# Kernel optimization log

Measured on AMD Instinct MI355X. Metric: run time of the kernel, lower is better.

## Reference

```python
import jax, jax.numpy as jnp
import numpy as np

N = 50000      # nodes
E = 800000     # edges
CIN = 128
CH = 128
COUT = 64
EPS = 1e-5     # BatchNorm eps


def setup_inputs() -> dict:
    key = jax.random.key(0)
    ks = jax.random.split(key, 16)
    s = 0.1  # weight scale for numerical stability
    return {
        "x": jax.random.normal(ks[0], (N, CIN), jnp.float32),
        "edge_index": jax.random.randint(ks[1], (2, E), 0, N, jnp.int32),
        "edge_weights": jax.random.uniform(ks[2], (E,), jnp.float32),
        "w1": jax.random.normal(ks[3], (CIN, CH), jnp.float32) * s,
        "b1": jnp.zeros((CH,), jnp.float32),
        "bn1_g": jnp.ones((CH,), jnp.float32),
        "bn1_b": jnp.zeros((CH,), jnp.float32),
        "bn1_m": jax.random.normal(ks[4], (CH,), jnp.float32) * 0.1,
        "bn1_v": jax.random.uniform(ks[5], (CH,), jnp.float32) + 0.5,
        "conv_ws": jax.random.normal(ks[6], (2, CH, CH), jnp.float32) * s,
        "conv_bs": jnp.zeros((2, CH), jnp.float32),
        "bns_g": jnp.ones((2, CH), jnp.float32),
        "bns_b": jnp.zeros((2, CH), jnp.float32),
        "bns_m": jax.random.normal(ks[7], (2, CH), jnp.float32) * 0.1,
        "bns_v": jax.random.uniform(ks[8], (2, CH), jnp.float32) + 0.5,
        "lin1_w": jax.random.normal(ks[9], (CH, CH), jnp.float32) * s,
        "lin1_b": jnp.zeros((CH,), jnp.float32),
        "lin2_w": jax.random.normal(ks[10], (CH, COUT), jnp.float32) * s,
        "lin2_b": jnp.zeros((COUT,), jnp.float32),
    }


def _bn(h, g, b, m, v):
    # BatchNorm1d in eval mode: running statistics
    return (h - m) * jax.lax.rsqrt(v + EPS) * g + b


def _gcn(h, w, b, src, dst, norm, n):
    # GCNConv: out[dst] += norm_e * (h @ W)[src]  (self loops already in src/dst)
    h = h @ w
    msg = h[src] * norm[:, None]                 # [E+N, CH]
    return jax.ops.segment_sum(msg, dst, num_segments=n) + b


def reference(x, edge_index, edge_weights, w1, b1, bn1_g, bn1_b, bn1_m, bn1_v,
              conv_ws, conv_bs, bns_g, bns_b, bns_m, bns_v,
              lin1_w, lin1_b, lin2_w, lin2_b):
    n = x.shape[0]
    loop = jnp.arange(n, dtype=edge_index.dtype)
    src = jnp.concatenate([edge_index[0], loop])
    dst = jnp.concatenate([edge_index[1], loop])
    ew = jnp.concatenate([edge_weights, jnp.ones((n,), edge_weights.dtype)])
    # symmetric degree normalization (PyG gcn_norm)
    deg = jax.ops.segment_sum(ew, dst, num_segments=n)
    dis = jnp.where(deg > 0, jax.lax.rsqrt(deg), 0.0)
    norm = dis[src] * ew * dis[dst]

    lrelu = jax.nn.leaky_relu  # slope 0.01, matches F.leaky_relu default
    h = lrelu(_bn(_gcn(x, w1, b1, src, dst, norm, n), bn1_g, bn1_b, bn1_m, bn1_v))
    for i in range(conv_ws.shape[0]):
        h = lrelu(_bn(_gcn(h, conv_ws[i], conv_bs[i], src, dst, norm, n),
                      bns_g[i], bns_b[i], bns_m[i], bns_v[i]) + h)
    h = lrelu(h @ lin1_w + lin1_b)
    # dropout is identity in eval mode
    return h @ lin2_w + lin2_b
```

## Files before the change

kernel.cpp:

```cpp
#include <hip/hip_runtime.h>
#include <hip/hip_bf16.h>


constexpr int   NN    = 50000;
constexpr int   EE    = 800000;
constexpr int   CH    = 128;
constexpr int   SLOTS = 64;
constexpr int   NBUK  = 782;
constexpr int   RCAP  = 2048;
constexpr int   EPB   = 4096;
constexpr float EPS   = 1e-5f;

typedef __attribute__((ext_vector_type(8))) short bf16x8;
typedef __attribute__((ext_vector_type(4))) float f32x4;
typedef unsigned long long u64;
typedef unsigned short u16;

__device__ inline u16 f2bf_rne(float f) {
  unsigned u = __float_as_uint(f);
  unsigned r = u + 0x7fffu + ((u >> 16) & 1u);
  return (u16)(r >> 16);
}
__device__ inline float bf2f(unsigned h16) {
  return __uint_as_float(h16 << 16);
}


__global__ __launch_bounds__(256) void bin_kernel(const int* __restrict__ ei,
                                                  const float* __restrict__ ew,
                                                  unsigned* __restrict__ gcur,
                                                  u64* __restrict__ bins) {
  __shared__ unsigned cnt[NBUK];
  __shared__ unsigned base[NBUK];
  const int tid = threadIdx.x;
  for (int b = tid; b < NBUK; b += 256) cnt[b] = 0;
  __syncthreads();
  const int e0 = blockIdx.x * EPB;
  unsigned pk[16]; u16 bkt[16]; u16 rnk[16]; unsigned char dl[16];
  #pragma unroll
  for (int i = 0; i < 16; i++) {
    int e = e0 + i * 256 + tid;
    if (e < EE) {
      int s = ei[e], d = ei[EE + e];
      float w = ew[e];
      bkt[i] = (u16)(d >> 6);
      dl[i]  = (unsigned char)(d & 63);
      pk[i]  = ((unsigned)f2bf_rne(w) << 16) | (unsigned)s;
      rnk[i] = (u16)atomicAdd(&cnt[bkt[i]], 1u);
    } else bkt[i] = 0xffffu;
  }
  __syncthreads();
  for (int b = tid; b < NBUK; b += 256) {
    unsigned c = cnt[b];
    base[b] = c ? atomicAdd(&gcur[b * 16], c) : 0u;
  }
  __syncthreads();
  #pragma unroll
  for (int i = 0; i < 16; i++) {
    if (bkt[i] == 0xffffu) continue;
    unsigned pos = base[bkt[i]] + rnk[i];
    if (pos < RCAP)
      bins[(size_t)bkt[i] * RCAP + pos] = ((u64)dl[i] << 32) | pk[i];
  }
}


__global__ __launch_bounds__(256) void scatter_kernel(const unsigned* __restrict__ gcur,
                                                      const u64* __restrict__ bins,
                                                      unsigned* __restrict__ ell,
                                                      float* __restrict__ dis) {
  __shared__ unsigned rank[64];
  __shared__ float    wsum[64];
  const int b   = blockIdx.x;
  const int tid = threadIdx.x;
  if (tid < 64) { rank[tid] = 1u; wsum[tid] = 0.f; }
  __syncthreads();
  unsigned cnt = gcur[b * 16];
  if (cnt > RCAP) cnt = RCAP;
  const u64* src = bins + (size_t)b * RCAP;
  for (unsigned i = tid; i < cnt; i += 256) {
    u64 v = src[i];
    unsigned pk = (unsigned)v;
    unsigned dl = (unsigned)(v >> 32);
    unsigned r = atomicAdd(&rank[dl], 1u);
    if (r < SLOTS)
      ell[((size_t)(b * 64 + dl)) * SLOTS + r] = pk;
    atomicAdd(&wsum[dl], bf2f(pk >> 16));
  }
  __syncthreads();
  if (tid < 64) {
    int node = b * 64 + tid;
    if (node < NN) {
      unsigned c = rank[tid];
      if (c > SLOTS) c = SLOTS;
      ell[(size_t)node * SLOTS] = c;
      dis[node] = rsqrtf(1.0f + wsum[tid]);
    }
  }
}

constexpr int NB_WZ = (73728 + 384 + 255) / 256;

__global__ void wswz_kernel(
    const float* __restrict__ w1, const float* __restrict__ bn1_g, const float* __restrict__ bn1_v,
    const float* __restrict__ conv_ws, const float* __restrict__ bns_g, const float* __restrict__ bns_v,
    const float* __restrict__ lin1_w, const float* __restrict__ lin2_w,
    const float* __restrict__ b1, const float* __restrict__ bn1_b, const float* __restrict__ bn1_m,
    const float* __restrict__ conv_bs, const float* __restrict__ bns_b, const float* __restrict__ bns_m,
    u16* __restrict__ w1h, u16* __restrict__ w1l,
    u16* __restrict__ c0h, u16* __restrict__ c0l,
    u16* __restrict__ c1h, u16* __restrict__ c1l,
    u16* __restrict__ l1h, u16* __restrict__ l1l,
    u16* __restrict__ l2h, u16* __restrict__ l2l,
    float* __restrict__ beff)
{
  int idx = blockIdx.x * 256 + threadIdx.x;
  if (idx >= 73728) {
    int r = idx - 73728;
    if (r >= 384) return;
    int l = r >> 7, c = r & 127;
    float bc, gg, bb, mm, vv;
    if (l == 0) { bc = b1[c]; gg = bn1_g[c]; bb = bn1_b[c]; mm = bn1_m[c]; vv = bn1_v[c]; }
    else {
      int o = (l - 1) * 128 + c;
      bc = conv_bs[o]; gg = bns_g[o]; bb = bns_b[o]; mm = bns_m[o]; vv = bns_v[o];
    }
    beff[r] = (bc - mm) * gg * rsqrtf(vv + EPS) + bb;
    return;
  }
  const float* W; const float* g = nullptr; const float* v = nullptr;
  u16 *hi, *lo; int CO = 128; int local;
  if      (idx < 16384) { W = w1;              g = bn1_g;     v = bn1_v;     hi = w1h; lo = w1l; local = idx; }
  else if (idx < 32768) { W = conv_ws;         g = bns_g;     v = bns_v;     hi = c0h; lo = c0l; local = idx - 16384; }
  else if (idx < 49152) { W = conv_ws + 16384; g = bns_g+128; v = bns_v+128; hi = c1h; lo = c1l; local = idx - 32768; }
  else if (idx < 65536) { W = lin1_w;                                        hi = l1h; lo = l1l; local = idx - 49152; }
  else                  { W = lin2_w;                                        hi = l2h; lo = l2l; local = idx - 65536; CO = 64; }
  int k = local / CO, n = local % CO;
  float w = W[local];
  if (g) w *= g[n] * rsqrtf(v[n] + EPS);
  int NCT = CO / 16;
  int kchunk = k >> 5, kin = k & 31, quad = kin >> 3, j = kin & 7;
  int ct = n >> 4, l = (quad << 4) | (n & 15);
  size_t pos = ((size_t)(kchunk * NCT + ct) * 64 + l) * 8 + j;
  u16 h = f2bf_rne(w);
  hi[pos] = h;
  lo[pos] = f2bf_rne(w - bf2f(h));
}

__global__ __launch_bounds__(256) void gemm1_kernel(
    const float* __restrict__ Ain,
    const u16* __restrict__ Whi, const u16* __restrict__ Wlo,
    const float* __restrict__ dis, u16* __restrict__ Cout)
{
  __shared__ float lds[64][CH + 4];
  const int tid  = threadIdx.x;
  const int wave = tid >> 6;
  const int lane = tid & 63;
  const int quad = lane >> 4;
  const int mrow = lane & 15;
  const int row0 = blockIdx.x * 64;

  int arow = row0 + wave * 16 + mrow;
  if (arow >= NN) arow = NN - 1;

  bf16x8 ahi[4], alo[4];
  const float* Ar = Ain + (size_t)arow * CH;
  #pragma unroll
  for (int c = 0; c < 4; c++) {
    int off = c * 32 + quad * 8;
    float4 f0 = *(const float4*)(Ar + off);
    float4 f1 = *(const float4*)(Ar + off + 4);
    float f[8] = {f0.x, f0.y, f0.z, f0.w, f1.x, f1.y, f1.z, f1.w};
    #pragma unroll
    for (int j = 0; j < 8; j++) {
      u16 h = f2bf_rne(f[j]);
      ahi[c][j] = (short)h;
      alo[c][j] = (short)f2bf_rne(f[j] - bf2f(h));
    }
  }

  f32x4 acc[8];
  #pragma unroll
  for (int t = 0; t < 8; t++) acc[t] = (f32x4){0.f, 0.f, 0.f, 0.f};
  #pragma unroll
  for (int c = 0; c < 4; c++) {
    #pragma unroll
    for (int t = 0; t < 8; t++) {
      size_t base = ((size_t)(c * 8 + t) * 64 + lane) * 8;
      bf16x8 bh = *(const bf16x8*)(Whi + base);
      bf16x8 bl = *(const bf16x8*)(Wlo + base);
      acc[t] = __builtin_amdgcn_mfma_f32_16x16x32_bf16(ahi[c], bh, acc[t], 0, 0, 0);
      acc[t] = __builtin_amdgcn_mfma_f32_16x16x32_bf16(alo[c], bh, acc[t], 0, 0, 0);
      acc[t] = __builtin_amdgcn_mfma_f32_16x16x32_bf16(ahi[c], bl, acc[t], 0, 0, 0);
    }
  }

  #pragma unroll
  for (int t = 0; t < 8; t++)
    #pragma unroll
    for (int r = 0; r < 4; r++)
      lds[wave * 16 + quad * 4 + r][t * 16 + mrow] = acc[t][r];
  __syncthreads();

  #pragma unroll
  for (int i = tid; i < 64 * CH / 4; i += 256) {
    int row = (i * 4) / CH;
    int col = (i * 4) % CH;
    int grow = row0 + row;
    if (grow >= NN) continue;
    float rs = dis[grow];
    const float* lp = &lds[row][col];
    u16* cp = (u16*)Cout + (size_t)grow * CH + col;
    unsigned p0 = ((unsigned)f2bf_rne(lp[1] * rs) << 16) | f2bf_rne(lp[0] * rs);
    unsigned p1 = ((unsigned)f2bf_rne(lp[3] * rs) << 16) | f2bf_rne(lp[2] * rs);
    *(uint2*)cp = make_uint2(p0, p1);
  }
}

template<bool RES>
__global__ __launch_bounds__(256, 5) void fuse_kernel(
    const u16* __restrict__ hwin,
    const unsigned* __restrict__ ell, const float* __restrict__ dis,
    const float* __restrict__ beff, const u16* __restrict__ res,
    const u16* __restrict__ Whi, const u16* __restrict__ Wlo,
    u16* __restrict__ hout, u16* __restrict__ hwout)
{
  __shared__ unsigned hs[64][68];
  const int tid  = threadIdx.x;
  const int wave = tid >> 6;
  const int lane = tid & 63;
  const int sub  = lane & 15;
  const int grp  = lane >> 4;
  const int row0 = blockIdx.x * 64;

  for (int r = 0; r < 16; r++) {
    int node = row0 + wave * 16 + r;
    int nd = node < NN ? node : NN - 1;
    unsigned myword = ell[(size_t)nd * SLOTS + lane];
    int cnt = __shfl((int)myword, 0);
    if (cnt > SLOTS) cnt = SLOTS;
    float a[8] = {0.f, 0.f, 0.f, 0.f, 0.f, 0.f, 0.f, 0.f};
    for (int j = 0; j < cnt; j += 16) {
      unsigned sidx[4]; float wv[4];
      #pragma unroll
      for (int q = 0; q < 4; q++) {
        int jj = j + q * 4 + grp;
        unsigned e = (unsigned)__shfl((int)myword, jj & 63);
        float    w = (jj == 0) ? 1.0f : bf2f(e >> 16);
        unsigned s = (jj == 0) ? (unsigned)nd : (e & 0xffffu);
        if (jj >= cnt) { w = 0.f; s = (unsigned)nd; }
        sidx[q] = s; wv[q] = w;
      }
      uint4 h[4];
      #pragma unroll
      for (int q = 0; q < 4; q++)
        h[q] = *(const uint4*)(hwin + (size_t)sidx[q] * CH + sub * 8);
      #pragma unroll
      for (int q = 0; q < 4; q++) {
        float w = wv[q];
        a[0] = fmaf(w, bf2f(h[q].x & 0xffffu), a[0]); a[1] = fmaf(w, bf2f(h[q].x >> 16), a[1]);
        a[2] = fmaf(w, bf2f(h[q].y & 0xffffu), a[2]); a[3] = fmaf(w, bf2f(h[q].y >> 16), a[3]);
        a[4] = fmaf(w, bf2f(h[q].z & 0xffffu), a[4]); a[5] = fmaf(w, bf2f(h[q].z >> 16), a[5]);
        a[6] = fmaf(w, bf2f(h[q].w & 0xffffu), a[6]); a[7] = fmaf(w, bf2f(h[q].w >> 16), a[7]);
      }
    }
    #pragma unroll
    for (int k = 0; k < 8; k++) {
      a[k] += __shfl_xor(a[k], 16);
      a[k] += __shfl_xor(a[k], 32);
    }
    if (grp == 0) {
      float disd = dis[nd];
      int c = sub * 8;
      float4 be0 = *(const float4*)(beff + c);
      float4 be1 = *(const float4*)(beff + c + 4);
      float y[8];
      y[0] = a[0] * disd + be0.x; y[1] = a[1] * disd + be0.y;
      y[2] = a[2] * disd + be0.z; y[3] = a[3] * disd + be0.w;
      y[4] = a[4] * disd + be1.x; y[5] = a[5] * disd + be1.y;
      y[6] = a[6] * disd + be1.z; y[7] = a[7] * disd + be1.w;
      if constexpr (RES) {
        uint4 rr = *(const uint4*)(res + (size_t)nd * CH + c);
        y[0] += bf2f(rr.x & 0xffffu); y[1] += bf2f(rr.x >> 16);
        y[2] += bf2f(rr.y & 0xffffu); y[3] += bf2f(rr.y >> 16);
        y[4] += bf2f(rr.z & 0xffffu); y[5] += bf2f(rr.z >> 16);
        y[6] += bf2f(rr.w & 0xffffu); y[7] += bf2f(rr.w >> 16);
      }
      #pragma unroll
      for (int k = 0; k < 8; k++) y[k] = y[k] > 0.f ? y[k] : 0.01f * y[k];
      uint4 o;
      o.x = ((unsigned)f2bf_rne(y[1]) << 16) | f2bf_rne(y[0]);
      o.y = ((unsigned)f2bf_rne(y[3]) << 16) | f2bf_rne(y[2]);
      o.z = ((unsigned)f2bf_rne(y[5]) << 16) | f2bf_rne(y[4]);
      o.w = ((unsigned)f2bf_rne(y[7]) << 16) | f2bf_rne(y[6]);
      if (node < NN) *(uint4*)(hout + (size_t)node * CH + c) = o;
      *(uint4*)&hs[wave * 16 + r][sub * 4] = o;
    }
  }

  bf16x8 af[4];
  #pragma unroll
  for (int c = 0; c < 4; c++)
    af[c] = *(const bf16x8*)&hs[wave * 16 + sub][c * 16 + grp * 4];

  f32x4 acc[8];
  #pragma unroll
  for (int t = 0; t < 8; t++) acc[t] = (f32x4){0.f, 0.f, 0.f, 0.f};
  #pragma unroll
  for (int c = 0; c < 4; c++) {
    #pragma unroll
    for (int t = 0; t < 8; t++) {
      size_t base = ((size_t)(c * 8 + t) * 64 + lane) * 8;
      bf16x8 bh = *(const bf16x8*)(Whi + base);
      bf16x8 bl = *(const bf16x8*)(Wlo + base);
      acc[t] = __builtin_amdgcn_mfma_f32_16x16x32_bf16(af[c], bh, acc[t], 0, 0, 0);
      acc[t] = __builtin_amdgcn_mfma_f32_16x16x32_bf16(af[c], bl, acc[t], 0, 0, 0);
    }
  }

  #pragma unroll
  for (int r = 0; r < 4; r++) {
    int grow = row0 + wave * 16 + grp * 4 + r;
    if (grow >= NN) continue;
    float rs = dis[grow];
    #pragma unroll
    for (int t = 0; t < 8; t++)
      hwout[(size_t)grow * CH + t * 16 + sub] = f2bf_rne(acc[t][r] * rs);
  }
}

__global__ __launch_bounds__(256, 4) void fuse_last_kernel(
    const u16* __restrict__ hwin,
    const unsigned* __restrict__ ell, const float* __restrict__ dis,
    const float* __restrict__ beff, const u16* __restrict__ res,
    const u16* __restrict__ l1h, const u16* __restrict__ l1l,
    const float* __restrict__ b1,
    const u16* __restrict__ l2h, const u16* __restrict__ l2l,
    const float* __restrict__ b2, float* __restrict__ out)
{
  __shared__ unsigned smem[64 * 132];
  float* fs = (float*)smem;
  const int tid  = threadIdx.x;
  const int wave = tid >> 6;
  const int lane = tid & 63;
  const int sub  = lane & 15;
  const int grp  = lane >> 4;
  const int row0 = blockIdx.x * 64;

  for (int r = 0; r < 16; r++) {
    int node = row0 + wave * 16 + r;
    int nd = node < NN ? node : NN - 1;
    unsigned myword = ell[(size_t)nd * SLOTS + lane];
    int cnt = __shfl((int)myword, 0);
    if (cnt > SLOTS) cnt = SLOTS;
    float a[8] = {0.f, 0.f, 0.f, 0.f, 0.f, 0.f, 0.f, 0.f};
    for (int j = 0; j < cnt; j += 16) {
      unsigned sidx[4]; float wv[4];
      #pragma unroll
      for (int q = 0; q < 4; q++) {
        int jj = j + q * 4 + grp;
        unsigned e = (unsigned)__shfl((int)myword, jj & 63);
        float    w = (jj == 0) ? 1.0f : bf2f(e >> 16);
        unsigned s = (jj == 0) ? (unsigned)nd : (e & 0xffffu);
        if (jj >= cnt) { w = 0.f; s = (unsigned)nd; }
        sidx[q] = s; wv[q] = w;
      }
      uint4 h[4];
      #pragma unroll
      for (int q = 0; q < 4; q++)
        h[q] = *(const uint4*)(hwin + (size_t)sidx[q] * CH + sub * 8);
      #pragma unroll
      for (int q = 0; q < 4; q++) {
        float w = wv[q];
        a[0] = fmaf(w, bf2f(h[q].x & 0xffffu), a[0]); a[1] = fmaf(w, bf2f(h[q].x >> 16), a[1]);
        a[2] = fmaf(w, bf2f(h[q].y & 0xffffu), a[2]); a[3] = fmaf(w, bf2f(h[q].y >> 16), a[3]);
        a[4] = fmaf(w, bf2f(h[q].z & 0xffffu), a[4]); a[5] = fmaf(w, bf2f(h[q].z >> 16), a[5]);
        a[6] = fmaf(w, bf2f(h[q].w & 0xffffu), a[6]); a[7] = fmaf(w, bf2f(h[q].w >> 16), a[7]);
      }
    }
    #pragma unroll
    for (int k = 0; k < 8; k++) {
      a[k] += __shfl_xor(a[k], 16);
      a[k] += __shfl_xor(a[k], 32);
    }
    if (grp == 0) {
      float disd = dis[nd];
      int c = sub * 8;
      float4 be0 = *(const float4*)(beff + c);
      float4 be1 = *(const float4*)(beff + c + 4);
      float y[8];
      y[0] = a[0] * disd + be0.x; y[1] = a[1] * disd + be0.y;
      y[2] = a[2] * disd + be0.z; y[3] = a[3] * disd + be0.w;
      y[4] = a[4] * disd + be1.x; y[5] = a[5] * disd + be1.y;
      y[6] = a[6] * disd + be1.z; y[7] = a[7] * disd + be1.w;
      uint4 rr = *(const uint4*)(res + (size_t)nd * CH + c);
      y[0] += bf2f(rr.x & 0xffffu); y[1] += bf2f(rr.x >> 16);
      y[2] += bf2f(rr.y & 0xffffu); y[3] += bf2f(rr.y >> 16);
      y[4] += bf2f(rr.z & 0xffffu); y[5] += bf2f(rr.z >> 16);
      y[6] += bf2f(rr.w & 0xffffu); y[7] += bf2f(rr.w >> 16);
      #pragma unroll
      for (int k = 0; k < 8; k++) y[k] = y[k] > 0.f ? y[k] : 0.01f * y[k];
      uint4 o;
      o.x = ((unsigned)f2bf_rne(y[1]) << 16) | f2bf_rne(y[0]);
      o.y = ((unsigned)f2bf_rne(y[3]) << 16) | f2bf_rne(y[2]);
      o.z = ((unsigned)f2bf_rne(y[5]) << 16) | f2bf_rne(y[4]);
      o.w = ((unsigned)f2bf_rne(y[7]) << 16) | f2bf_rne(y[6]);
      *(uint4*)&smem[(wave * 16 + r) * 68 + sub * 4] = o;
    }
  }

  bf16x8 af[4];
  #pragma unroll
  for (int c = 0; c < 4; c++)
    af[c] = *(const bf16x8*)&smem[(wave * 16 + sub) * 68 + c * 16 + grp * 4];
  __syncthreads();

  f32x4 acc[8];
  #pragma unroll
  for (int t = 0; t < 8; t++) acc[t] = (f32x4){0.f, 0.f, 0.f, 0.f};
  #pragma unroll
  for (int c = 0; c < 4; c++) {
    #pragma unroll
    for (int t = 0; t < 8; t++) {
      size_t base = ((size_t)(c * 8 + t) * 64 + lane) * 8;
      bf16x8 bh = *(const bf16x8*)(l1h + base);
      bf16x8 bl = *(const bf16x8*)(l1l + base);
      acc[t] = __builtin_amdgcn_mfma_f32_16x16x32_bf16(af[c], bh, acc[t], 0, 0, 0);
      acc[t] = __builtin_amdgcn_mfma_f32_16x16x32_bf16(af[c], bl, acc[t], 0, 0, 0);
    }
  }
  #pragma unroll
  for (int t = 0; t < 8; t++) {
    float bb = b1[t * 16 + sub];
    #pragma unroll
    for (int r = 0; r < 4; r++) {
      float x = acc[t][r] + bb;
      x = x > 0.f ? x : 0.01f * x;
      fs[(wave * 16 + grp * 4 + r) * 132 + t * 16 + sub] = x;
    }
  }

  f32x4 acc2[4];
  #pragma unroll
  for (int t = 0; t < 4; t++) acc2[t] = (f32x4){0.f, 0.f, 0.f, 0.f};
  #pragma unroll
  for (int c = 0; c < 4; c++) {
    bf16x8 ahi, alo;
    const float* lp = &fs[(wave * 16 + sub) * 132 + c * 32 + grp * 8];
    float4 f0 = *(const float4*)lp;
    float4 f1 = *(const float4*)(lp + 4);
    float f[8] = {f0.x, f0.y, f0.z, f0.w, f1.x, f1.y, f1.z, f1.w};
    #pragma unroll
    for (int j = 0; j < 8; j++) {
      u16 h = f2bf_rne(f[j]);
      ahi[j] = (short)h;
      alo[j] = (short)f2bf_rne(f[j] - bf2f(h));
    }
    #pragma unroll
    for (int t = 0; t < 4; t++) {
      size_t base = ((size_t)(c * 4 + t) * 64 + lane) * 8;
      bf16x8 bh = *(const bf16x8*)(l2h + base);
      bf16x8 bl = *(const bf16x8*)(l2l + base);
      acc2[t] = __builtin_amdgcn_mfma_f32_16x16x32_bf16(ahi, bh, acc2[t], 0, 0, 0);
      acc2[t] = __builtin_amdgcn_mfma_f32_16x16x32_bf16(alo, bh, acc2[t], 0, 0, 0);
      acc2[t] = __builtin_amdgcn_mfma_f32_16x16x32_bf16(ahi, bl, acc2[t], 0, 0, 0);
    }
  }
  #pragma unroll
  for (int t = 0; t < 4; t++) {
    float bb = b2[t * 16 + sub];
    #pragma unroll
    for (int r = 0; r < 4; r++) {
      int grow = row0 + wave * 16 + grp * 4 + r;
      if (grow < NN)
        out[(size_t)grow * 64 + t * 16 + sub] = acc2[t][r] + bb;
    }
  }
}


extern "C" void kernel_launch(void* const* d_in, const int* in_sizes, int n_in,
                              void* d_out, int out_size, void* d_ws, size_t ws_size,
                              hipStream_t stream) {
  const float* x       = (const float*)d_in[0];
  const int*   ei      = (const int*)  d_in[1];
  const float* ew      = (const float*)d_in[2];
  const float* w1      = (const float*)d_in[3];
  const float* b1      = (const float*)d_in[4];
  const float* bn1_g   = (const float*)d_in[5];
  const float* bn1_b   = (const float*)d_in[6];
  const float* bn1_m   = (const float*)d_in[7];
  const float* bn1_v   = (const float*)d_in[8];
  const float* conv_ws = (const float*)d_in[9];
  const float* conv_bs = (const float*)d_in[10];
  const float* bns_g   = (const float*)d_in[11];
  const float* bns_b   = (const float*)d_in[12];
  const float* bns_m   = (const float*)d_in[13];
  const float* bns_v   = (const float*)d_in[14];
  const float* lin1_w  = (const float*)d_in[15];
  const float* lin1_b  = (const float*)d_in[16];
  const float* lin2_w  = (const float*)d_in[17];
  const float* lin2_b  = (const float*)d_in[18];
  float* out = (float*)d_out;

  size_t off = 0;
  auto alloc = [&](size_t elems) -> void* {
    void* p = (char*)d_ws + off * 4;
    off += (elems + 3) & ~(size_t)3;
    return p;
  };
  unsigned* gcur = (unsigned*)alloc(NBUK * 16);
  u64*      bins = (u64*)     alloc((size_t)NBUK * RCAP * 2);
  unsigned* ell  = (unsigned*)alloc((size_t)NN * SLOTS);
  float*    dis  = (float*)   alloc(NN);
  float*    beff = (float*)   alloc(3 * CH);
  u16*      hwa  = (u16*)     alloc((size_t)NN * CH / 2);
  u16*      hwb  = (u16*)     alloc((size_t)NN * CH / 2);
  u16*      h1   = (u16*)     alloc((size_t)NN * CH / 2);
  u16*      h2   = (u16*)     alloc((size_t)NN * CH / 2);
  u16* w1h = (u16*)alloc(CH * CH / 2); u16* w1l = (u16*)alloc(CH * CH / 2);
  u16* c0h = (u16*)alloc(CH * CH / 2); u16* c0l = (u16*)alloc(CH * CH / 2);
  u16* c1h = (u16*)alloc(CH * CH / 2); u16* c1l = (u16*)alloc(CH * CH / 2);
  u16* l1h = (u16*)alloc(CH * CH / 2); u16* l1l = (u16*)alloc(CH * CH / 2);
  u16* l2h = (u16*)alloc(CH * 64 / 2); u16* l2l = (u16*)alloc(CH * 64 / 2);

  const int nb_bin  = (EE + EPB - 1) / EPB;
  const int nb_gemm = (NN + 63) / 64;
  dim3 B(256);

  hipMemsetAsync(gcur, 0, NBUK * 16 * sizeof(unsigned), stream);
  bin_kernel    <<<nb_bin, B, 0, stream>>>(ei, ew, gcur, bins);
  scatter_kernel<<<NBUK,   B, 0, stream>>>(gcur, bins, ell, dis);

  wswz_kernel<<<NB_WZ, B, 0, stream>>>(w1, bn1_g, bn1_v, conv_ws, bns_g, bns_v,
      lin1_w, lin2_w, b1, bn1_b, bn1_m, conv_bs, bns_b, bns_m,
      w1h, w1l, c0h, c0l, c1h, c1l, l1h, l1l, l2h, l2l, beff);

  gemm1_kernel<<<nb_gemm, B, 0, stream>>>(x, w1h, w1l, dis, hwa);

  fuse_kernel<false><<<nb_gemm, B, 0, stream>>>(hwa, ell, dis, beff, nullptr,
      c0h, c0l, h1, hwb);

  fuse_kernel<true><<<nb_gemm, B, 0, stream>>>(hwb, ell, dis, beff + CH, h1,
      c1h, c1l, h2, hwa);

  fuse_last_kernel<<<nb_gemm, B, 0, stream>>>(hwa, ell, dis, beff + 2 * CH, h2,
      l1h, l1l, lin1_b, l2h, l2l, lin2_b, out);
}
```

Before: 314.2 us.

## Switch to CSR adjacency and channel-sliced feature layout with split aggregate/GEMM kernels

Replaces the fixed 64-slot ELL adjacency with a compact CSR built through a new prefix-scan kernel. Features are stored in 8 channel slices of 16 bf16 each, so each aggregation block gathers a 32-byte slice per neighbour and the working set per slice is small enough to sit in cache. The fused aggregate+GEMM kernels are split into separate sagg, sgemm and linf kernels. This adds launches and extra global round trips for intermediates, in exchange for better gather locality and higher parallelism.

```diff
diff --git a/kernel.cpp b/kernel.cpp
--- a/kernel.cpp
+++ b/kernel.cpp
@@ -5,7 +5,6 @@
 constexpr int   NN    = 50000;
 constexpr int   EE    = 800000;
 constexpr int   CH    = 128;
-constexpr int   SLOTS = 64;
 constexpr int   NBUK  = 782;
 constexpr int   RCAP  = 2048;
 constexpr int   EPB   = 4096;
@@ -65,37 +64,80 @@
 }
 
 
+__global__ __launch_bounds__(256) void scan_kernel(const unsigned* __restrict__ gcur,
+                                                   unsigned* __restrict__ bbase) {
+  __shared__ unsigned lds[256];
+  __shared__ unsigned carry;
+  if (threadIdx.x == 0) carry = 0;
+  __syncthreads();
+  for (int base = 0; base < NBUK; base += 256) {
+    int i = base + threadIdx.x;
+    unsigned v = 0;
+    if (i < NBUK) { v = gcur[i * 16]; if (v > RCAP) v = RCAP; }
+    lds[threadIdx.x] = v;
+    __syncthreads();
+    for (int off = 1; off < 256; off <<= 1) {
+      unsigned t = (threadIdx.x >= off) ? lds[threadIdx.x - off] : 0u;
+      __syncthreads();
+      lds[threadIdx.x] += t;
+      __syncthreads();
+    }
+    if (i < NBUK) bbase[i] = carry + lds[threadIdx.x] - v;
+    __syncthreads();
+    if (threadIdx.x == 255) carry += lds[255];
+    __syncthreads();
+  }
+}
+
+
 __global__ __launch_bounds__(256) void scatter_kernel(const unsigned* __restrict__ gcur,
                                                       const u64* __restrict__ bins,
-                                                      unsigned* __restrict__ ell,
+                                                      const unsigned* __restrict__ bbase,
+                                                      unsigned* __restrict__ hdr,
+                                                      unsigned* __restrict__ edges,
                                                       float* __restrict__ dis) {
   __shared__ unsigned rank[64];
   __shared__ float    wsum[64];
+  __shared__ unsigned noff[64];
+  __shared__ unsigned rank2[64];
   const int b   = blockIdx.x;
   const int tid = threadIdx.x;
-  if (tid < 64) { rank[tid] = 1u; wsum[tid] = 0.f; }
+  if (tid < 64) { rank[tid] = 0u; wsum[tid] = 0.f; rank2[tid] = 0u; }
   __syncthreads();
   unsigned cnt = gcur[b * 16];
   if (cnt > RCAP) cnt = RCAP;
   const u64* src = bins + (size_t)b * RCAP;
   for (unsigned i = tid; i < cnt; i += 256) {
     u64 v = src[i];
-    unsigned pk = (unsigned)v;
     unsigned dl = (unsigned)(v >> 32);
-    unsigned r = atomicAdd(&rank[dl], 1u);
-    if (r < SLOTS)
-      ell[((size_t)(b * 64 + dl)) * SLOTS + r] = pk;
-    atomicAdd(&wsum[dl], bf2f(pk >> 16));
+    atomicAdd(&rank[dl], 1u);
+    atomicAdd(&wsum[dl], bf2f(((unsigned)v) >> 16));
+  }
+  __syncthreads();
+  if (tid == 0) {
+    unsigned acc = bbase[b];
+    #pragma unroll 1
+    for (int k = 0; k < 64; k++) {
+      noff[k] = acc;
+      unsigned c = rank[k]; if (c > 63u) c = 63u;
+      acc += c;
+    }
   }
   __syncthreads();
   if (tid < 64) {
     int node = b * 64 + tid;
     if (node < NN) {
-      unsigned c = rank[tid];
-      if (c > SLOTS) c = SLOTS;
-      ell[(size_t)node * SLOTS] = c;
+      unsigned c = rank[tid]; if (c > 63u) c = 63u;
+      hdr[node] = (noff[tid] << 6) | c;
       dis[node] = rsqrtf(1.0f + wsum[tid]);
     }
+  }
+  __syncthreads();
+  for (unsigned i = tid; i < cnt; i += 256) {
+    u64 v = src[i];
+    unsigned dl = (unsigned)(v >> 32);
+    unsigned r = atomicAdd(&rank2[dl], 1u);
+    if (r < 63u) edges[noff[dl] + r] = (unsigned)v;
   }
 }
 
@@ -202,76 +244,81 @@
       lds[wave * 16 + quad * 4 + r][t * 16 + mrow] = acc[t][r];
   __syncthreads();
 
-  #pragma unroll
-  for (int i = tid; i < 64 * CH / 4; i += 256) {
-    int row = (i * 4) / CH;
-    int col = (i * 4) % CH;
+  for (int i = tid; i < 64 * 8; i += 256) {
+    int row = i >> 3, slice = i & 7;
     int grow = row0 + row;
     if (grow >= NN) continue;
     float rs = dis[grow];
-    const float* lp = &lds[row][col];
-    u16* cp = (u16*)Cout + (size_t)grow * CH + col;
-    unsigned p0 = ((unsigned)f2bf_rne(lp[1] * rs) << 16) | f2bf_rne(lp[0] * rs);
-    unsigned p1 = ((unsigned)f2bf_rne(lp[3] * rs) << 16) | f2bf_rne(lp[2] * rs);
-    *(uint2*)cp = make_uint2(p0, p1);
+    const float* lp = &lds[row][slice * 16];
+    u16* cp = Cout + ((size_t)slice * NN + grow) * 16;
+    uint4 o0, o1;
+    o0.x = ((unsigned)f2bf_rne(lp[1] * rs) << 16) | f2bf_rne(lp[0] * rs);
+    o0.y = ((unsigned)f2bf_rne(lp[3] * rs) << 16) | f2bf_rne(lp[2] * rs);
+    o0.z = ((unsigned)f2bf_rne(lp[5] * rs) << 16) | f2bf_rne(lp[4] * rs);
+    o0.w = ((unsigned)f2bf_rne(lp[7] * rs) << 16) | f2bf_rne(lp[6] * rs);
+    o1.x = ((unsigned)f2bf_rne(lp[9] * rs) << 16) | f2bf_rne(lp[8] * rs);
+    o1.y = ((unsigned)f2bf_rne(lp[11] * rs) << 16) | f2bf_rne(lp[10] * rs);
+    o1.z = ((unsigned)f2bf_rne(lp[13] * rs) << 16) | f2bf_rne(lp[12] * rs);
+    o1.w = ((unsigned)f2bf_rne(lp[15] * rs) << 16) | f2bf_rne(lp[14] * rs);
+    *(uint4*)cp = o0;
+    *(uint4*)(cp + 8) = o1;
   }
 }
 
 template<bool RES>
-__global__ __launch_bounds__(256, 5) void fuse_kernel(
-    const u16* __restrict__ hwin,
-    const unsigned* __restrict__ ell, const float* __restrict__ dis,
+__global__ __launch_bounds__(256) void sagg_kernel(
+    const u16* __restrict__ hw, const unsigned* __restrict__ hdr,
+    const unsigned* __restrict__ edges, const float* __restrict__ dis,
     const float* __restrict__ beff, const u16* __restrict__ res,
-    const u16* __restrict__ Whi, const u16* __restrict__ Wlo,
-    u16* __restrict__ hout, u16* __restrict__ hwout)
+    u16* __restrict__ hout)
 {
-  __shared__ unsigned hs[64][68];
-  const int tid  = threadIdx.x;
-  const int wave = tid >> 6;
-  const int lane = tid & 63;
-  const int sub  = lane & 15;
-  const int grp  = lane >> 4;
-  const int row0 = blockIdx.x * 64;
+  const int blk   = blockIdx.x;
+  const int slice = blk & 7;
+  const int tile  = blk >> 3;
+  const int wave  = threadIdx.x >> 6;
+  const int lane  = threadIdx.x & 63;
+  const int half  = lane & 1;
+  const int eid   = lane >> 1;
+  const u16* hws  = hw + (size_t)slice * NN * 16;
 
   for (int r = 0; r < 16; r++) {
-    int node = row0 + wave * 16 + r;
+    int node = tile * 64 + wave * 16 + r;
     int nd = node < NN ? node : NN - 1;
-    unsigned myword = ell[(size_t)nd * SLOTS + lane];
-    int cnt = __shfl((int)myword, 0);
-    if (cnt > SLOTS) cnt = SLOTS;
+    unsigned h = hdr[nd];
+    unsigned off = h >> 6;
+    int cnt = (int)(h & 63u);
+
     float a[8] = {0.f, 0.f, 0.f, 0.f, 0.f, 0.f, 0.f, 0.f};
-    for (int j = 0; j < cnt; j += 16) {
-      unsigned sidx[4]; float wv[4];
-      #pragma unroll
-      for (int q = 0; q < 4; q++) {
-        int jj = j + q * 4 + grp;
-        unsigned e = (unsigned)__shfl((int)myword, jj & 63);
-        float    w = (jj == 0) ? 1.0f : bf2f(e >> 16);
-        unsigned s = (jj == 0) ? (unsigned)nd : (e & 0xffffu);
-        if (jj >= cnt) { w = 0.f; s = (unsigned)nd; }
-        sidx[q] = s; wv[q] = w;
+    for (int jb = 0; jb < cnt; jb += 32) {
+      int jj = jb + eid;
+      if (jj < cnt) {
+        unsigned e = edges[off + jj];
+        float w = bf2f(e >> 16);
+        unsigned s = e & 0xffffu;
+        uint4 hv = *(const uint4*)(hws + (size_t)s * 16 + half * 8);
+        a[0] = fmaf(w, bf2f(hv.x & 0xffffu), a[0]); a[1] = fmaf(w, bf2f(hv.x >> 16), a[1]);
+        a[2] = fmaf(w, bf2f(hv.y & 0xffffu), a[2]); a[3] = fmaf(w, bf2f(hv.y >> 16), a[3]);
+        a[4] = fmaf(w, bf2f(hv.z & 0xffffu), a[4]); a[5] = fmaf(w, bf2f(hv.z >> 16), a[5]);
+        a[6] = fmaf(w, bf2f(hv.w & 0xffffu), a[6]); a[7] = fmaf(w, bf2f(hv.w >> 16), a[7]);
       }
-      uint4 h[4];
-      #pragma unroll
-      for (int q = 0; q < 4; q++)
-        h[q] = *(const uint4*)(hwin + (size_t)sidx[q] * CH + sub * 8);
-      #pragma unroll
-      for (int q = 0; q < 4; q++) {
-        float w = wv[q];
-        a[0] = fmaf(w, bf2f(h[q].x & 0xffffu), a[0]); a[1] = fmaf(w, bf2f(h[q].x >> 16), a[1]);
-        a[2] = fmaf(w, bf2f(h[q].y & 0xffffu), a[2]); a[3] = fmaf(w, bf2f(h[q].y >> 16), a[3]);
-        a[4] = fmaf(w, bf2f(h[q].z & 0xffffu), a[4]); a[5] = fmaf(w, bf2f(h[q].z >> 16), a[5]);
-        a[6] = fmaf(w, bf2f(h[q].w & 0xffffu), a[6]); a[7] = fmaf(w, bf2f(h[q].w >> 16), a[7]);
-      }
     }
     #pragma unroll
     for (int k = 0; k < 8; k++) {
+      a[k] += __shfl_xor(a[k], 2);
+      a[k] += __shfl_xor(a[k], 4);
+      a[k] += __shfl_xor(a[k], 8);
       a[k] += __shfl_xor(a[k], 16);
       a[k] += __shfl_xor(a[k], 32);
     }
-    if (grp == 0) {
+
+    if (lane < 2 && node < NN) {
+      uint4 sv = *(const uint4*)(hws + (size_t)nd * 16 + half * 8);
+      a[0] += bf2f(sv.x & 0xffffu); a[1] += bf2f(sv.x >> 16);
+      a[2] += bf2f(sv.y & 0xffffu); a[3] += bf2f(sv.y >> 16);
+      a[4] += bf2f(sv.z & 0xffffu); a[5] += bf2f(sv.z >> 16);
+      a[6] += bf2f(sv.w & 0xffffu); a[7] += bf2f(sv.w >> 16);
       float disd = dis[nd];
-      int c = sub * 8;
+      int c = slice * 16 + half * 8;
       float4 be0 = *(const float4*)(beff + c);
       float4 be1 = *(const float4*)(beff + c + 4);
       float y[8];
@@ -280,7 +327,7 @@
       y[4] = a[4] * disd + be1.x; y[5] = a[5] * disd + be1.y;
       y[6] = a[6] * disd + be1.z; y[7] = a[7] * disd + be1.w;
       if constexpr (RES) {
-        uint4 rr = *(const uint4*)(res + (size_t)nd * CH + c);
+        uint4 rr = *(const uint4*)(res + ((size_t)slice * NN + nd) * 16 + half * 8);
         y[0] += bf2f(rr.x & 0xffffu); y[1] += bf2f(rr.x >> 16);
         y[2] += bf2f(rr.y & 0xffffu); y[3] += bf2f(rr.y >> 16);
         y[4] += bf2f(rr.z & 0xffffu); y[5] += bf2f(rr.z >> 16);
@@ -293,15 +340,33 @@
       o.y = ((unsigned)f2bf_rne(y[3]) << 16) | f2bf_rne(y[2]);
       o.z = ((unsigned)f2bf_rne(y[5]) << 16) | f2bf_rne(y[4]);
       o.w = ((unsigned)f2bf_rne(y[7]) << 16) | f2bf_rne(y[6]);
-      if (node < NN) *(uint4*)(hout + (size_t)node * CH + c) = o;
-      *(uint4*)&hs[wave * 16 + r][sub * 4] = o;
-    }
-  }
+      *(uint4*)(hout + ((size_t)slice * NN + node) * 16 + half * 8) = o;
+    }
+  }
+}
+
+__global__ __launch_bounds__(256) void sgemm_kernel(
+    const u16* __restrict__ Ain,
+    const u16* __restrict__ Whi, const u16* __restrict__ Wlo,
+    const float* __restrict__ dis, u16* __restrict__ Cout)
+{
+  const int tid  = threadIdx.x;
+  const int wave = tid >> 6;
+  const int lane = tid & 63;
+  const int quad = lane >> 4;
+  const int mrow = lane & 15;
+  const int row0 = blockIdx.x * 64;
+
+  int arow = row0 + wave * 16 + mrow;
+  if (arow >= NN) arow = NN - 1;
 
   bf16x8 af[4];
   #pragma unroll
-  for (int c = 0; c < 4; c++)
-    af[c] = *(const bf16x8*)&hs[wave * 16 + sub][c * 16 + grp * 4];
+  for (int c = 0; c < 4; c++) {
+    int slice = 2 * c + (quad >> 1);
+    int off = (quad & 1) * 8;
+    af[c] = *(const bf16x8*)(Ain + ((size_t)slice * NN + arow) * 16 + off);
+  }
 
   f32x4 acc[8];
   #pragma unroll
@@ -320,100 +385,40 @@
 
   #pragma unroll
   for (int r = 0; r < 4; r++) {
-    int grow = row0 + wave * 16 + grp * 4 + r;
+    int grow = row0 + wave * 16 + quad * 4 + r;
     if (grow >= NN) continue;
     float rs = dis[grow];
     #pragma unroll
     for (int t = 0; t < 8; t++)
-      hwout[(size_t)grow * CH + t * 16 + sub] = f2bf_rne(acc[t][r] * rs);
-  }
-}
-
-__global__ __launch_bounds__(256, 4) void fuse_last_kernel(
-    const u16* __restrict__ hwin,
-    const unsigned* __restrict__ ell, const float* __restrict__ dis,
-    const float* __restrict__ beff, const u16* __restrict__ res,
+      Cout[((size_t)t * NN + grow) * 16 + mrow] = f2bf_rne(acc[t][r] * rs);
+  }
+}
+
+__global__ __launch_bounds__(256) void linf_kernel(
+    const u16* __restrict__ Ain,
     const u16* __restrict__ l1h, const u16* __restrict__ l1l,
     const float* __restrict__ b1,
     const u16* __restrict__ l2h, const u16* __restrict__ l2l,
     const float* __restrict__ b2, float* __restrict__ out)
 {
-  __shared__ unsigned smem[64 * 132];
-  float* fs = (float*)smem;
+  __shared__ float fs[64 * 132];
   const int tid  = threadIdx.x;
   const int wave = tid >> 6;
   const int lane = tid & 63;
-  const int sub  = lane & 15;
-  const int grp  = lane >> 4;
+  const int quad = lane >> 4;
+  const int mrow = lane & 15;
   const int row0 = blockIdx.x * 64;
 
-  for (int r = 0; r < 16; r++) {
-    int node = row0 + wave * 16 + r;
-    int nd = node < NN ? node : NN - 1;
-    unsigned myword = ell[(size_t)nd * SLOTS + lane];
-    int cnt = __shfl((int)myword, 0);
-    if (cnt > SLOTS) cnt = SLOTS;
-    float a[8] = {0.f, 0.f, 0.f, 0.f, 0.f, 0.f, 0.f, 0.f};
-    for (int j = 0; j < cnt; j += 16) {
-      unsigned sidx[4]; float wv[4];
-      #pragma unroll
-      for (int q = 0; q < 4; q++) {
-        int jj = j + q * 4 + grp;
-        unsigned e = (unsigned)__shfl((int)myword, jj & 63);
-        float    w = (jj == 0) ? 1.0f : bf2f(e >> 16);
-        unsigned s = (jj == 0) ? (unsigned)nd : (e & 0xffffu);
-        if (jj >= cnt) { w = 0.f; s = (unsigned)nd; }
-        sidx[q] = s; wv[q] = w;
-      }
-      uint4 h[4];
-      #pragma unroll
-      for (int q = 0; q < 4; q++)
-        h[q] = *(const uint4*)(hwin + (size_t)sidx[q] * CH + sub * 8);
-      #pragma unroll
-      for (int q = 0; q < 4; q++) {
-        float w = wv[q];
-        a[0] = fmaf(w, bf2f(h[q].x & 0xffffu), a[0]); a[1] = fmaf(w, bf2f(h[q].x >> 16), a[1]);
-        a[2] = fmaf(w, bf2f(h[q].y & 0xffffu), a[2]); a[3] = fmaf(w, bf2f(h[q].y >> 16), a[3]);
-        a[4] = fmaf(w, bf2f(h[q].z & 0xffffu), a[4]); a[5] = fmaf(w, bf2f(h[q].z >> 16), a[5]);
-        a[6] = fmaf(w, bf2f(h[q].w & 0xffffu), a[6]); a[7] = fmaf(w, bf2f(h[q].w >> 16), a[7]);
-      }
-    }
-    #pragma unroll
-    for (int k = 0; k < 8; k++) {
-      a[k] += __shfl_xor(a[k], 16);
-      a[k] += __shfl_xor(a[k], 32);
-    }
-    if (grp == 0) {
-      float disd = dis[nd];
-      int c = sub * 8;
-      float4 be0 = *(const float4*)(beff + c);
-      float4 be1 = *(const float4*)(beff + c + 4);
-      float y[8];
-      y[0] = a[0] * disd + be0.x; y[1] = a[1] * disd + be0.y;
-      y[2] = a[2] * disd + be0.z; y[3] = a[3] * disd + be0.w;
-      y[4] = a[4] * disd + be1.x; y[5] = a[5] * disd + be1.y;
-      y[6] = a[6] * disd + be1.z; y[7] = a[7] * disd + be1.w;
-      uint4 rr = *(const uint4*)(res + (size_t)nd * CH + c);
-      y[0] += bf2f(rr.x & 0xffffu); y[1] += bf2f(rr.x >> 16);
-      y[2] += bf2f(rr.y & 0xffffu); y[3] += bf2f(rr.y >> 16);
-      y[4] += bf2f(rr.z & 0xffffu); y[5] += bf2f(rr.z >> 16);
-      y[6] += bf2f(rr.w & 0xffffu); y[7] += bf2f(rr.w >> 16);
-      #pragma unroll
-      for (int k = 0; k < 8; k++) y[k] = y[k] > 0.f ? y[k] : 0.01f * y[k];
-      uint4 o;
-      o.x = ((unsigned)f2bf_rne(y[1]) << 16) | f2bf_rne(y[0]);
-      o.y = ((unsigned)f2bf_rne(y[3]) << 16) | f2bf_rne(y[2]);
-      o.z = ((unsigned)f2bf_rne(y[5]) << 16) | f2bf_rne(y[4]);
-      o.w = ((unsigned)f2bf_rne(y[7]) << 16) | f2bf_rne(y[6]);
-      *(uint4*)&smem[(wave * 16 + r) * 68 + sub * 4] = o;
-    }
-  }
+  int arow = row0 + wave * 16 + mrow;
+  if (arow >= NN) arow = NN - 1;
 
   bf16x8 af[4];
   #pragma unroll
-  for (int c = 0; c < 4; c++)
-    af[c] = *(const bf16x8*)&smem[(wave * 16 + sub) * 68 + c * 16 + grp * 4];
-  __syncthreads();
+  for (int c = 0; c < 4; c++) {
+    int slice = 2 * c + (quad >> 1);
+    int off = (quad & 1) * 8;
+    af[c] = *(const bf16x8*)(Ain + ((size_t)slice * NN + arow) * 16 + off);
+  }
 
   f32x4 acc[8];
   #pragma unroll
@@ -431,12 +436,12 @@
   }
   #pragma unroll
   for (int t = 0; t < 8; t++) {
-    float bb = b1[t * 16 + sub];
+    float bb = b1[t * 16 + mrow];
     #pragma unroll
     for (int r = 0; r < 4; r++) {
       float x = acc[t][r] + bb;
       x = x > 0.f ? x : 0.01f * x;
-      fs[(wave * 16 + grp * 4 + r) * 132 + t * 16 + sub] = x;
+      fs[(wave * 16 + quad * 4 + r) * 132 + t * 16 + mrow] = x;
     }
   }
 
@@ -446,7 +451,7 @@
   #pragma unroll
   for (int c = 0; c < 4; c++) {
     bf16x8 ahi, alo;
-    const float* lp = &fs[(wave * 16 + sub) * 132 + c * 32 + grp * 8];
+    const float* lp = &fs[(wave * 16 + mrow) * 132 + c * 32 + quad * 8];
     float4 f0 = *(const float4*)lp;
     float4 f1 = *(const float4*)(lp + 4);
     float f[8] = {f0.x, f0.y, f0.z, f0.w, f1.x, f1.y, f1.z, f1.w};
@@ -468,12 +473,12 @@
   }
   #pragma unroll
   for (int t = 0; t < 4; t++) {
-    float bb = b2[t * 16 + sub];
+    float bb = b2[t * 16 + mrow];
     #pragma unroll
     for (int r = 0; r < 4; r++) {
-      int grow = row0 + wave * 16 + grp * 4 + r;
+      int grow = row0 + wave * 16 + quad * 4 + r;
       if (grow < NN)
-        out[(size_t)grow * 64 + t * 16 + sub] = acc2[t][r] + bb;
+        out[(size_t)grow * 64 + t * 16 + mrow] = acc2[t][r] + bb;
     }
   }
 }
@@ -509,15 +514,16 @@
     off += (elems + 3) & ~(size_t)3;
     return p;
   };
-  unsigned* gcur = (unsigned*)alloc(NBUK * 16);
-  u64*      bins = (u64*)     alloc((size_t)NBUK * RCAP * 2);
-  unsigned* ell  = (unsigned*)alloc((size_t)NN * SLOTS);
-  float*    dis  = (float*)   alloc(NN);
-  float*    beff = (float*)   alloc(3 * CH);
-  u16*      hwa  = (u16*)     alloc((size_t)NN * CH / 2);
-  u16*      hwb  = (u16*)     alloc((size_t)NN * CH / 2);
-  u16*      h1   = (u16*)     alloc((size_t)NN * CH / 2);
-  u16*      h2   = (u16*)     alloc((size_t)NN * CH / 2);
+  unsigned* gcur  = (unsigned*)alloc(NBUK * 16);
+  u64*      bins  = (u64*)     alloc((size_t)NBUK * RCAP * 2);
+  unsigned* bbase = (unsigned*)alloc(NBUK);
+  unsigned* hdr   = (unsigned*)alloc(NN);
+  unsigned* edges = (unsigned*)alloc(EE);
+  float*    dis   = (float*)   alloc(NN);
+  float*    beff  = (float*)   alloc(3 * CH);
+  u16*      hw    = (u16*)     alloc((size_t)NN * CH / 2);
+  u16*      hA    = (u16*)     alloc((size_t)NN * CH / 2);
+  u16*      hB    = (u16*)     alloc((size_t)NN * CH / 2);
   u16* w1h = (u16*)alloc(CH * CH / 2); u16* w1l = (u16*)alloc(CH * CH / 2);
   u16* c0h = (u16*)alloc(CH * CH / 2); u16* c0l = (u16*)alloc(CH * CH / 2);
   u16* c1h = (u16*)alloc(CH * CH / 2); u16* c1l = (u16*)alloc(CH * CH / 2);
@@ -525,25 +531,27 @@
   u16* l2h = (u16*)alloc(CH * 64 / 2); u16* l2l = (u16*)alloc(CH * 64 / 2);
 
   const int nb_bin  = (EE + EPB - 1) / EPB;
-  const int nb_gemm = (NN + 63) / 64;
+  const int nb_tile = (NN + 63) / 64;
+  const int nb_sagg = nb_tile * 8;
   dim3 B(256);
 
   hipMemsetAsync(gcur, 0, NBUK * 16 * sizeof(unsigned), stream);
   bin_kernel    <<<nb_bin, B, 0, stream>>>(ei, ew, gcur, bins);
-  scatter_kernel<<<NBUK,   B, 0, stream>>>(gcur, bins, ell, dis);
+  scan_kernel   <<<1,      B, 0, stream>>>(gcur, bbase);
+  scatter_kernel<<<NBUK,   B, 0, stream>>>(gcur, bins, bbase, hdr, edges, dis);
 
   wswz_kernel<<<NB_WZ, B, 0, stream>>>(w1, bn1_g, bn1_v, conv_ws, bns_g, bns_v,
       lin1_w, lin2_w, b1, bn1_b, bn1_m, conv_bs, bns_b, bns_m,
       w1h, w1l, c0h, c0l, c1h, c1l, l1h, l1l, l2h, l2l, beff);
 
-  gemm1_kernel<<<nb_gemm, B, 0, stream>>>(x, w1h, w1l, dis, hwa);
-
-  fuse_kernel<false><<<nb_gemm, B, 0, stream>>>(hwa, ell, dis, beff, nullptr,
-      c0h, c0l, h1, hwb);
-
-  fuse_kernel<true><<<nb_gemm, B, 0, stream>>>(hwb, ell, dis, beff + CH, h1,
-      c1h, c1l, h2, hwa);
-
-  fuse_last_kernel<<<nb_gemm, B, 0, stream>>>(hwa, ell, dis, beff + 2 * CH, h2,
-      l1h, l1l, lin1_b, l2h, l2l, lin2_b, out);
-}
+  gemm1_kernel<<<nb_tile, B, 0, stream>>>(x, w1h, w1l, dis, hw);
+  sagg_kernel<false><<<nb_sagg, B, 0, stream>>>(hw, hdr, edges, dis, beff, nullptr, hA);
+
+  sgemm_kernel<<<nb_tile, B, 0, stream>>>(hA, c0h, c0l, dis, hw);
+  sagg_kernel<true><<<nb_sagg, B, 0, stream>>>(hw, hdr, edges, dis, beff + CH, hA, hB);
+
+  sgemm_kernel<<<nb_tile, B, 0, stream>>>(hB, c1h, c1l, dis, hw);
+  sagg_kernel<true><<<nb_sagg, B, 0, stream>>>(hw, hdr, edges, dis, beff + 2 * CH, hB, hA);
+
+  linf_kernel<<<nb_tile, B, 0, stream>>>(hA, l1h, l1l, lin1_b, l2h, l2l, lin2_b, out);
+}
```

New measurement: 741.8 us. +136.1%, slower.
